# Kernel optimization log

Measured on AMD Instinct MI355X. Metric: run time of the kernel, lower is better.

## Reference

```python
import jax, jax.numpy as jnp
import numpy as np

N = 100000          # nodes
E = 1600000         # edges
NODE_DIM = 128
EDGE_DIM = 1
EMB = 16            # out_channels per head
H = 2               # heads
HID = 32
OUT = 2
NEG_SLOPE = 0.2


def gatv2_layer(x, src, dst, eattr, Wl, bl, Wr, br, We, att, bias):
    """PyG GATv2Conv: add self-loops (edge_attr fill='mean'), edge attention,
    segment softmax over target nodes, scatter-add aggregation, concat heads."""
    n = x.shape[0]
    heads, ch = att.shape
    # --- add self loops; self-loop edge_attr = mean of incoming edge_attr per node ---
    ones = jnp.ones((src.shape[0],), dtype=x.dtype)
    deg = jax.ops.segment_sum(ones, dst, num_segments=n)
    loop_attr = jax.ops.segment_sum(eattr, dst, num_segments=n) / jnp.maximum(deg, 1.0)[:, None]
    idx = jnp.arange(n, dtype=src.dtype)
    src2 = jnp.concatenate([src, idx])
    dst2 = jnp.concatenate([dst, idx])
    eattr2 = jnp.concatenate([eattr, loop_attr], axis=0)
    # --- linear projections ---
    xl = (x @ Wl + bl).reshape(n, heads, ch)   # source-side (lin_l)
    xr = (x @ Wr + br).reshape(n, heads, ch)   # target-side (lin_r)
    ef = (eattr2 @ We).reshape(-1, heads, ch)  # edge features (lin_edge, no bias)
    # --- per-edge attention logits (GATv2: LeakyReLU inside, then att dot) ---
    e = xl[src2] + xr[dst2] + ef               # [E2, H, C]
    e = jnp.where(e >= 0, e, NEG_SLOPE * e)
    logits = jnp.einsum('ehc,hc->eh', e, att)  # [E2, H]
    # --- segment softmax over edges sharing the same target node ---
    m = jax.ops.segment_max(logits, dst2, num_segments=n)      # [N, H]
    a = jnp.exp(logits - m[dst2])
    denom = jax.ops.segment_sum(a, dst2, num_segments=n)
    alpha = a / denom[dst2]                                    # [E2, H]
    # --- scatter-add weighted source messages ---
    msg = (alpha[:, :, None] * xl[src2]).reshape(-1, heads * ch)
    out = jax.ops.segment_sum(msg, dst2, num_segments=n)       # [N, H*C]
    return out + bias


def setup_inputs() -> dict:
    key = jax.random.key(0)
    ks = jax.random.split(key, 24)
    p = lambda k, s: (jax.random.normal(k, s, dtype=jnp.float32) * 0.1)
    HC = H * EMB
    return {
        'x': jax.random.normal(ks[0], (N, NODE_DIM), dtype=jnp.float32),
        'edge_index': jax.random.randint(ks[1], (2, E), 0, N, dtype=jnp.int32),
        'edge_attr': jax.random.normal(ks[2], (E, EDGE_DIM), dtype=jnp.float32),
        # layer 1
        'Wl1': p(ks[3], (NODE_DIM, HC)), 'bl1': p(ks[4], (HC,)),
        'Wr1': p(ks[5], (NODE_DIM, HC)), 'br1': p(ks[6], (HC,)),
        'We1': p(ks[7], (EDGE_DIM, HC)), 'att1': p(ks[8], (H, EMB)), 'b1': p(ks[9], (HC,)),
        # layer 2 (input dim = H*EMB)
        'Wl2': p(ks[10], (HC, HC)), 'bl2': p(ks[11], (HC,)),
        'Wr2': p(ks[12], (HC, HC)), 'br2': p(ks[13], (HC,)),
        'We2': p(ks[14], (EDGE_DIM, HC)), 'att2': p(ks[15], (H, EMB)), 'b2': p(ks[16], (HC,)),
        # decoder MLP
        'Wd1': p(ks[17], (HC, HID)), 'bd1': p(ks[18], (HID,)),
        'Wd2': p(ks[19], (HID, OUT)), 'bd2': p(ks[20], (OUT,)),
    }


def reference(x, edge_index, edge_attr,
              Wl1, bl1, Wr1, br1, We1, att1, b1,
              Wl2, bl2, Wr2, br2, We2, att2, b2,
              Wd1, bd1, Wd2, bd2):
    src, dst = edge_index[0], edge_index[1]
    h = gatv2_layer(x, src, dst, edge_attr, Wl1, bl1, Wr1, br1, We1, att1, b1)
    h = gatv2_layer(h, src, dst, edge_attr, Wl2, bl2, Wr2, br2, We2, att2, b2)
    h = jax.nn.relu(h @ Wd1 + bd1)
    return h @ Wd2 + bd2
```

## Files before the change

kernel.cpp:

```cpp
#include <hip/hip_runtime.h>
#include <hip/hip_fp16.h>
#include <math.h>


#define NN 100000
#define NE 1600000
#define SLOT 48
#define ROWU 64
#define NEG_SLOPE 0.2f

__device__ __forceinline__ float pk_ea(unsigned p) {
    return __half2float(__ushort_as_half((unsigned short)((p & 0x7FFFu) << 1)));
}
__device__ __forceinline__ float lrelu(float v) {
    return (v >= 0.f) ? v : NEG_SLOPE * v;
}

__device__ __forceinline__ void scatter_chunk(int bid, int tid,
                                              const int* __restrict__ src,
                                              const int* __restrict__ dst,
                                              const float* __restrict__ eattr,
                                              unsigned* __restrict__ csr) {
#pragma unroll
    for (int i = 0; i < 2; i++) {
        int e = bid * 512 + i * 256 + tid;
        int d = dst[e];
        unsigned* row = csr + (size_t)d * ROWU;
        int pos = atomicAdd((int*)row, 1);
        if (pos < SLOT) {
            unsigned hb = __half_as_ushort(__float2half_rn(eattr[e]));
            row[4 + pos] = ((unsigned)src[e] << 15) | (hb >> 1);
        }
    }
}

template <int K>
__global__ void proj_scatter_kernel(const float* __restrict__ x,
                                    const float* __restrict__ Wl, const float* __restrict__ bl,
                                    const float* __restrict__ Wr, const float* __restrict__ br,
                                    __half* __restrict__ xl, float* __restrict__ xr,
                                    const int* __restrict__ src, const int* __restrict__ dst,
                                    const float* __restrict__ eattr,
                                    unsigned* __restrict__ csr) {
    __shared__ __align__(16) float sWl[K * 32];
    __shared__ __align__(16) float sWr[K * 32];
    __shared__ float sb[64];
    bool scat_first = (blockIdx.x & 1) != 0;
    if (scat_first)
        scatter_chunk(blockIdx.x, threadIdx.x, src, dst, eattr, csr);
    for (int a = threadIdx.x; a < K * 32; a += blockDim.x) {
        int col = a / K, p = a % K;
        int k = (((p >> 2) ^ (col & 7)) << 2) | (p & 3);
        sWl[a] = Wl[k * 32 + col];
        sWr[a] = Wr[k * 32 + col];
    }
    if (threadIdx.x < 32) sb[threadIdx.x] = bl[threadIdx.x];
    else if (threadIdx.x < 64) sb[threadIdx.x] = br[threadIdx.x - 32];
    __syncthreads();
    int t = blockIdx.x * blockDim.x + threadIdx.x;
    int g = t >> 5, col = t & 31;
    int row0 = g * 4;
    {
        const float4* x0 = (const float4*)(x + (size_t)(row0 + 0) * K);
        const float4* x1 = (const float4*)(x + (size_t)(row0 + 1) * K);
        const float4* x2 = (const float4*)(x + (size_t)(row0 + 2) * K);
        const float4* x3 = (const float4*)(x + (size_t)(row0 + 3) * K);
        const float4* wl4 = (const float4*)(sWl + col * K);
        const float4* wr4 = (const float4*)(sWr + col * K);
        int swz = col & 7;
        float al0 = 0.f, al1 = 0.f, al2 = 0.f, al3 = 0.f;
        float ar0 = 0.f, ar1 = 0.f, ar2 = 0.f, ar3 = 0.f;
#pragma unroll 4
        for (int k4 = 0; k4 < K / 4; k4++) {
            float4 wl = wl4[k4 ^ swz];
            float4 wr = wr4[k4 ^ swz];
            float4 a = x0[k4];
            float4 b = x1[k4];
            float4 c = x2[k4];
            float4 d = x3[k4];
            al0 = fmaf(a.x, wl.x, al0); al0 = fmaf(a.y, wl.y, al0);
            al0 = fmaf(a.z, wl.z, al0); al0 = fmaf(a.w, wl.w, al0);
            ar0 = fmaf(a.x, wr.x, ar0); ar0 = fmaf(a.y, wr.y, ar0);
            ar0 = fmaf(a.z, wr.z, ar0); ar0 = fmaf(a.w, wr.w, ar0);
            al1 = fmaf(b.x, wl.x, al1); al1 = fmaf(b.y, wl.y, al1);
            al1 = fmaf(b.z, wl.z, al1); al1 = fmaf(b.w, wl.w, al1);
            ar1 = fmaf(b.x, wr.x, ar1); ar1 = fmaf(b.y, wr.y, ar1);
            ar1 = fmaf(b.z, wr.z, ar1); ar1 = fmaf(b.w, wr.w, ar1);
            al2 = fmaf(c.x, wl.x, al2); al2 = fmaf(c.y, wl.y, al2);
            al2 = fmaf(c.z, wl.z, al2); al2 = fmaf(c.w, wl.w, al2);
            ar2 = fmaf(c.x, wr.x, ar2); ar2 = fmaf(c.y, wr.y, ar2);
            ar2 = fmaf(c.z, wr.z, ar2); ar2 = fmaf(c.w, wr.w, ar2);
            al3 = fmaf(d.x, wl.x, al3); al3 = fmaf(d.y, wl.y, al3);
            al3 = fmaf(d.z, wl.z, al3); al3 = fmaf(d.w, wl.w, al3);
            ar3 = fmaf(d.x, wr.x, ar3); ar3 = fmaf(d.y, wr.y, ar3);
            ar3 = fmaf(d.w, wr.w, ar3); ar3 = fmaf(d.z, wr.z, ar3);
        }
        float bls = sb[col], brs = sb[32 + col];
        xl[(size_t)(row0 + 0) * 32 + col] = __float2half_rn(al0 + bls);
        xr[(size_t)(row0 + 0) * 32 + col] = ar0 + brs;
        xl[(size_t)(row0 + 1) * 32 + col] = __float2half_rn(al1 + bls);
        xr[(size_t)(row0 + 1) * 32 + col] = ar1 + brs;
        xl[(size_t)(row0 + 2) * 32 + col] = __float2half_rn(al2 + bls);
        xr[(size_t)(row0 + 2) * 32 + col] = ar2 + brs;
        xl[(size_t)(row0 + 3) * 32 + col] = __float2half_rn(al3 + bls);
        xr[(size_t)(row0 + 3) * 32 + col] = ar3 + brs;
    }
    if (!scat_first)
        scatter_chunk(blockIdx.x, threadIdx.x, src, dst, eattr, csr);
}

__device__ __forceinline__ void gat_core4(const unsigned* __restrict__ csr,
                                          const __half* xl, const float* xr,
                                          const float* We, const float* att,
                                          const float* bias, int node, int L,
                                          float h[4]) {
    int k = L & 7, j = L >> 3;
    const unsigned* row = csr + (size_t)node * ROWU;
    int cnt = (int)row[0];
    int deg = (cnt < SLOT) ? cnt : SLOT;
    float4 we = ((const float4*)We)[k];
    float4 at = ((const float4*)att)[k];
    float4 xrc = ((const float4*)(xr + (size_t)node * 32))[k];
    ushort4 sq = ((const ushort4*)(xl + (size_t)node * 32))[k];
    float sx0 = __half2float(__ushort_as_half(sq.x));
    float sx1 = __half2float(__ushort_as_half(sq.y));
    float sx2 = __half2float(__ushort_as_half(sq.z));
    float sx3 = __half2float(__ushort_as_half(sq.w));
    float ssum = 0.f, a0 = 0.f, a1 = 0.f, a2 = 0.f, a3 = 0.f, easum = 0.f;
    unsigned pv_c = row[4 + j];
    int n1 = j + 4; if (n1 > SLOT - 1) n1 = SLOT - 1;
    unsigned pv_n = row[4 + n1];
    bool val_c = j < deg;
    int s_c = val_c ? (int)(pv_c >> 15) : 0;
    ushort4 q_c = ((const ushort4*)(xl + (size_t)s_c * 32))[k];
    for (int base = 0; base < deg; base += 4) {
        int idx = base + j;
        bool val_n = (idx + 4) < deg;
        int s_n = val_n ? (int)(pv_n >> 15) : 0;
        ushort4 q_n = ((const ushort4*)(xl + (size_t)s_n * 32))[k];
        int n2 = idx + 8; if (n2 > SLOT - 1) n2 = SLOT - 1;
        unsigned pv_n2 = row[4 + n2];
        float ea = pk_ea(pv_c);
        float x0 = __half2float(__ushort_as_half(q_c.x));
        float x1 = __half2float(__ushort_as_half(q_c.y));
        float x2 = __half2float(__ushort_as_half(q_c.z));
        float x3 = __half2float(__ushort_as_half(q_c.w));
        float p;
        p  = at.x * lrelu(fmaf(ea, we.x, x0 + xrc.x));
        p  = fmaf(at.y, lrelu(fmaf(ea, we.y, x1 + xrc.y)), p);
        p  = fmaf(at.z, lrelu(fmaf(ea, we.z, x2 + xrc.z)), p);
        p  = fmaf(at.w, lrelu(fmaf(ea, we.w, x3 + xrc.w)), p);
        p += __shfl_xor(p, 1);
        p += __shfl_xor(p, 2);
        float w = val_c ? __expf(p) : 0.f;
        ssum += w;
        easum += val_c ? ea : 0.f;
        a0 = fmaf(w, x0, a0);
        a1 = fmaf(w, x1, a1);
        a2 = fmaf(w, x2, a2);
        a3 = fmaf(w, x3, a3);
        pv_c = pv_n; pv_n = pv_n2; q_c = q_n; val_c = val_n;
    }
    ssum  += __shfl_xor(ssum, 8);   ssum  += __shfl_xor(ssum, 16);
    easum += __shfl_xor(easum, 8);  easum += __shfl_xor(easum, 16);
    a0 += __shfl_xor(a0, 8);  a0 += __shfl_xor(a0, 16);
    a1 += __shfl_xor(a1, 8);  a1 += __shfl_xor(a1, 16);
    a2 += __shfl_xor(a2, 8);  a2 += __shfl_xor(a2, 16);
    a3 += __shfl_xor(a3, 8);  a3 += __shfl_xor(a3, 16);
    {
        float ea0 = easum / fmaxf((float)cnt, 1.f);
        float p;
        p  = at.x * lrelu(fmaf(ea0, we.x, sx0 + xrc.x));
        p  = fmaf(at.y, lrelu(fmaf(ea0, we.y, sx1 + xrc.y)), p);
        p  = fmaf(at.z, lrelu(fmaf(ea0, we.z, sx2 + xrc.z)), p);
        p  = fmaf(at.w, lrelu(fmaf(ea0, we.w, sx3 + xrc.w)), p);
        p += __shfl_xor(p, 1);
        p += __shfl_xor(p, 2);
        float w = __expf(p);
        ssum += w;
        a0 = fmaf(w, sx0, a0);
        a1 = fmaf(w, sx1, a1);
        a2 = fmaf(w, sx2, a2);
        a3 = fmaf(w, sx3, a3);
    }
    float4 bq = ((const float4*)bias)[k];
    float inv = 1.f / ssum;
    h[0] = a0 * inv + bq.x;
    h[1] = a1 * inv + bq.y;
    h[2] = a2 * inv + bq.z;
    h[3] = a3 * inv + bq.w;
}

#define HBUF_FENCE() do { \
    asm volatile("s_waitcnt lgkmcnt(0)" ::: "memory"); \
    __builtin_amdgcn_sched_barrier(0); \
} while (0)

__global__ void gat1_proj2_kernel(const unsigned* __restrict__ csr,
                                  const __half* __restrict__ xl, const float* __restrict__ xr,
                                  const float* __restrict__ We, const float* __restrict__ att,
                                  const float* __restrict__ bias,
                                  const float* __restrict__ Wl2, const float* __restrict__ bl2,
                                  const float* __restrict__ Wr2, const float* __restrict__ br2,
                                  __half* __restrict__ xl2, float* __restrict__ xr2) {
    __shared__ __align__(16) float sWl[1024];
    __shared__ __align__(16) float sWr[1024];
    __shared__ float4 hbuf[8][8];
    for (int i = threadIdx.x; i < 1024; i += blockDim.x) {
        int cc = i >> 5, Lc = i & 31;
        int p = (((cc >> 2) ^ (Lc & 7)) << 2) | (cc & 3);
        sWl[Lc * 32 + p] = Wl2[i];
        sWr[Lc * 32 + p] = Wr2[i];
    }
    __syncthreads();
    int t = blockIdx.x * blockDim.x + threadIdx.x;
    int node = t >> 5, L = t & 31;
    if (node >= NN) return;
    float h[4];
    gat_core4(csr, xl, xr, We, att, bias, node, L, h);
    int nl = threadIdx.x >> 5;
    if (L < 8) hbuf[nl][L] = make_float4(h[0], h[1], h[2], h[3]);
    HBUF_FENCE();
    const float4* hv4 = hbuf[nl];
    const float4* wl4 = (const float4*)(sWl + L * 32);
    const float4* wr4 = (const float4*)(sWr + L * 32);
    int swz = L & 7;
    float al = bl2[L], ar = br2[L];
#pragma unroll
    for (int c4 = 0; c4 < 8; c4++) {
        float4 hv = hv4[c4];
        float4 wl = wl4[c4 ^ swz];
        float4 wr = wr4[c4 ^ swz];
        al = fmaf(hv.x, wl.x, al); al = fmaf(hv.y, wl.y, al);
        al = fmaf(hv.z, wl.z, al); al = fmaf(hv.w, wl.w, al);
        ar = fmaf(hv.x, wr.x, ar); ar = fmaf(hv.y, wr.y, ar);
        ar = fmaf(hv.z, wr.z, ar); ar = fmaf(hv.w, wr.w, ar);
    }
    xl2[(size_t)node * 32 + L] = __float2half_rn(al);
    xr2[(size_t)node * 32 + L] = ar;
}

__global__ void gat2_dec_kernel(const unsigned* __restrict__ csr,
                                const __half* __restrict__ xl, const float* __restrict__ xr,
                                const float* __restrict__ We, const float* __restrict__ att,
                                const float* __restrict__ bias,
                                const float* __restrict__ Wd1, const float* __restrict__ bd1,
                                const float* __restrict__ Wd2, const float* __restrict__ bd2,
                                float* __restrict__ out) {
    __shared__ __align__(16) float sWd1[1024];
    __shared__ float sWd2[64];
    __shared__ float4 hbuf[8][8];
    for (int i = threadIdx.x; i < 1024; i += blockDim.x) {
        int cc = i >> 5, Lc = i & 31;
        int p = (((cc >> 2) ^ (Lc & 7)) << 2) | (cc & 3);
        sWd1[Lc * 32 + p] = Wd1[i];
    }
    if (threadIdx.x < 64) sWd2[threadIdx.x] = Wd2[threadIdx.x];
    __syncthreads();
    int t = blockIdx.x * blockDim.x + threadIdx.x;
    int node = t >> 5, L = t & 31;
    if (node >= NN) return;
    float h[4];
    gat_core4(csr, xl, xr, We, att, bias, node, L, h);
    int nl = threadIdx.x >> 5;
    if (L < 8) hbuf[nl][L] = make_float4(h[0], h[1], h[2], h[3]);
    HBUF_FENCE();
    const float4* hv4 = hbuf[nl];
    const float4* wd4 = (const float4*)(sWd1 + L * 32);
    int swz = L & 7;
    float d1 = bd1[L];
#pragma unroll
    for (int c4 = 0; c4 < 8; c4++) {
        float4 hv = hv4[c4];
        float4 wd = wd4[c4 ^ swz];
        d1 = fmaf(hv.x, wd.x, d1); d1 = fmaf(hv.y, wd.y, d1);
        d1 = fmaf(hv.z, wd.z, d1); d1 = fmaf(hv.w, wd.w, d1);
    }
    float hid = fmaxf(d1, 0.f);
    float o0 = hid * sWd2[L * 2 + 0];
    float o1 = hid * sWd2[L * 2 + 1];
    o0 += __shfl_xor(o0, 1);   o1 += __shfl_xor(o1, 1);
    o0 += __shfl_xor(o0, 2);   o1 += __shfl_xor(o1, 2);
    o0 += __shfl_xor(o0, 4);   o1 += __shfl_xor(o1, 4);
    o0 += __shfl_xor(o0, 8);   o1 += __shfl_xor(o1, 8);
    o0 += __shfl_xor(o0, 16);  o1 += __shfl_xor(o1, 16);
    if (L == 0) {
        out[(size_t)node * 2 + 0] = o0 + bd2[0];
        out[(size_t)node * 2 + 1] = o1 + bd2[1];
    }
}

extern "C" void kernel_launch(void* const* d_in, const int* in_sizes, int n_in,
                              void* d_out, int out_size, void* d_ws, size_t ws_size,
                              hipStream_t stream) {
    const float* x     = (const float*)d_in[0];
    const int*   src   = (const int*)d_in[1];
    const int*   dst   = src + NE;
    const float* eattr = (const float*)d_in[2];
    const float* Wl1 = (const float*)d_in[3],  *bl1 = (const float*)d_in[4];
    const float* Wr1 = (const float*)d_in[5],  *br1 = (const float*)d_in[6];
    const float* We1 = (const float*)d_in[7],  *att1 = (const float*)d_in[8];
    const float* b1  = (const float*)d_in[9];
    const float* Wl2 = (const float*)d_in[10], *bl2 = (const float*)d_in[11];
    const float* Wr2 = (const float*)d_in[12], *br2 = (const float*)d_in[13];
    const float* We2 = (const float*)d_in[14], *att2 = (const float*)d_in[15];
    const float* b2  = (const float*)d_in[16];
    const float* Wd1 = (const float*)d_in[17], *bd1 = (const float*)d_in[18];
    const float* Wd2 = (const float*)d_in[19], *bd2 = (const float*)d_in[20];
    float* out = (float*)d_out;

    char* w = (char*)d_ws;
    unsigned* csr = (unsigned*)w;  w += (size_t)NN * ROWU * 4;
    __half*   xl  = (__half*)w;    w += (size_t)NN * 32 * 2;
    float*    xr  = (float*)w;     w += (size_t)NN * 32 * 4;
    __half*   xl2 = (__half*)w;    w += (size_t)NN * 32 * 2;
    float*    xr2 = (float*)w;     w += (size_t)NN * 32 * 4;

    const int B = 256;
    const int gN32 = (NN * 32) / B;
    const int gP   = (NN / 4 * 32) / B;

    hipMemsetAsync(csr, 0, (size_t)NN * ROWU * 4, stream);

    proj_scatter_kernel<128><<<gP, B, 0, stream>>>(x, Wl1, bl1, Wr1, br1, xl, xr,
                                                   src, dst, eattr, csr);

    gat1_proj2_kernel<<<gN32, B, 0, stream>>>(csr, xl, xr, We1, att1, b1,
                                              Wl2, bl2, Wr2, br2, xl2, xr2);

    gat2_dec_kernel<<<gN32, B, 0, stream>>>(csr, xl2, xr2, We2, att2, b2,
                                            Wd1, bd1, Wd2, bd2, out);
}
```

Measured before the change: 390.1 us.

## Use full 64-lane wave per node in first GAT layer aggregation

The first GAT layer now assigns 64 lanes per node instead of 32, so eight edges are processed in parallel per iteration with prefetching of the next source rows. The second-layer projection is split so half the wave computes lin_l and half lin_r. The projection kernel also always runs the edge scatter after the matmul and replaces div/mod with shifts. This aims to raise memory-level parallelism on the gather-heavy aggregation, at the cost of more shuffle reductions and fewer nodes per block.

```diff
diff --git a/kernel.cpp b/kernel.cpp
--- a/kernel.cpp
+++ b/kernel.cpp
@@ -45,11 +45,8 @@
     __shared__ __align__(16) float sWl[K * 32];
     __shared__ __align__(16) float sWr[K * 32];
     __shared__ float sb[64];
-    bool scat_first = (blockIdx.x & 1) != 0;
-    if (scat_first)
-        scatter_chunk(blockIdx.x, threadIdx.x, src, dst, eattr, csr);
     for (int a = threadIdx.x; a < K * 32; a += blockDim.x) {
-        int col = a / K, p = a % K;
+        int col = a >> 7, p = a & (K - 1);
         int k = (((p >> 2) ^ (col & 7)) << 2) | (p & 3);
         sWl[a] = Wl[k * 32 + col];
         sWr[a] = Wr[k * 32 + col];
@@ -105,8 +102,89 @@
         xl[(size_t)(row0 + 3) * 32 + col] = __float2half_rn(al3 + bls);
         xr[(size_t)(row0 + 3) * 32 + col] = ar3 + brs;
     }
-    if (!scat_first)
-        scatter_chunk(blockIdx.x, threadIdx.x, src, dst, eattr, csr);
+    scatter_chunk(blockIdx.x, threadIdx.x, src, dst, eattr, csr);
+}
+
+__device__ __forceinline__ void gat_core8(const unsigned* __restrict__ csr,
+                                          const __half* xl, const float* xr,
+                                          const float* We, const float* att,
+                                          const float* bias, int node, int L,
+                                          float h[4]) {
+    int k = L & 7, j = L >> 3;
+    const unsigned* row = csr + (size_t)node * ROWU;
+    int cnt = (int)row[0];
+    int deg = (cnt < SLOT) ? cnt : SLOT;
+    float4 we = ((const float4*)We)[k];
+    float4 at = ((const float4*)att)[k];
+    float4 xrc = ((const float4*)(xr + (size_t)node * 32))[k];
+    ushort4 sq = ((const ushort4*)(xl + (size_t)node * 32))[k];
+    float sx0 = __half2float(__ushort_as_half(sq.x));
+    float sx1 = __half2float(__ushort_as_half(sq.y));
+    float sx2 = __half2float(__ushort_as_half(sq.z));
+    float sx3 = __half2float(__ushort_as_half(sq.w));
+    float ssum = 0.f, a0 = 0.f, a1 = 0.f, a2 = 0.f, a3 = 0.f, easum = 0.f;
+    unsigned pv_c = row[4 + j];
+    int n1 = j + 8; if (n1 > SLOT - 1) n1 = SLOT - 1;
+    unsigned pv_n = row[4 + n1];
+    bool val_c = j < deg;
+    int s_c = val_c ? (int)(pv_c >> 15) : 0;
+    ushort4 q_c = ((const ushort4*)(xl + (size_t)s_c * 32))[k];
+    for (int base = 0; base < deg; base += 8) {
+        int idx = base + j;
+        bool val_n = (idx + 8) < deg;
+        int s_n = val_n ? (int)(pv_n >> 15) : 0;
+        ushort4 q_n = ((const ushort4*)(xl + (size_t)s_n * 32))[k];
+        int n2 = idx + 16; if (n2 > SLOT - 1) n2 = SLOT - 1;
+        unsigned pv_n2 = row[4 + n2];
+        float ea = pk_ea(pv_c);
+        float x0 = __half2float(__ushort_as_half(q_c.x));
+        float x1 = __half2float(__ushort_as_half(q_c.y));
+        float x2 = __half2float(__ushort_as_half(q_c.z));
+        float x3 = __half2float(__ushort_as_half(q_c.w));
+        float p;
+        p  = at.x * lrelu(fmaf(ea, we.x, x0 + xrc.x));
+        p  = fmaf(at.y, lrelu(fmaf(ea, we.y, x1 + xrc.y)), p);
+        p  = fmaf(at.z, lrelu(fmaf(ea, we.z, x2 + xrc.z)), p);
+        p  = fmaf(at.w, lrelu(fmaf(ea, we.w, x3 + xrc.w)), p);
+        p += __shfl_xor(p, 1);
+        p += __shfl_xor(p, 2);
+        float w = val_c ? __expf(p) : 0.f;
+        ssum += w;
+        easum += val_c ? ea : 0.f;
+        a0 = fmaf(w, x0, a0);
+        a1 = fmaf(w, x1, a1);
+        a2 = fmaf(w, x2, a2);
+        a3 = fmaf(w, x3, a3);
+        pv_c = pv_n; pv_n = pv_n2; q_c = q_n; val_c = val_n;
+    }
+    ssum  += __shfl_xor(ssum, 8);   ssum  += __shfl_xor(ssum, 16);  ssum  += __shfl_xor(ssum, 32);
+    easum += __shfl_xor(easum, 8);  easum += __shfl_xor(easum, 16); easum += __shfl_xor(easum, 32);
+    a0 += __shfl_xor(a0, 8);  a0 += __shfl_xor(a0, 16);  a0 += __shfl_xor(a0, 32);
+    a1 += __shfl_xor(a1, 8);  a1 += __shfl_xor(a1, 16);  a1 += __shfl_xor(a1, 32);
+    a2 += __shfl_xor(a2, 8);  a2 += __shfl_xor(a2, 16);  a2 += __shfl_xor(a2, 32);
+    a3 += __shfl_xor(a3, 8);  a3 += __shfl_xor(a3, 16);  a3 += __shfl_xor(a3, 32);
+    {
+        float ea0 = easum / fmaxf((float)cnt, 1.f);
+        float p;
+        p  = at.x * lrelu(fmaf(ea0, we.x, sx0 + xrc.x));
+        p  = fmaf(at.y, lrelu(fmaf(ea0, we.y, sx1 + xrc.y)), p);
+        p  = fmaf(at.z, lrelu(fmaf(ea0, we.z, sx2 + xrc.z)), p);
+        p  = fmaf(at.w, lrelu(fmaf(ea0, we.w, sx3 + xrc.w)), p);
+        p += __shfl_xor(p, 1);
+        p += __shfl_xor(p, 2);
+        float w = __expf(p);
+        ssum += w;
+        a0 = fmaf(w, sx0, a0);
+        a1 = fmaf(w, sx1, a1);
+        a2 = fmaf(w, sx2, a2);
+        a3 = fmaf(w, sx3, a3);
+    }
+    float4 bq = ((const float4*)bias)[k];
+    float inv = 1.f / ssum;
+    h[0] = a0 * inv + bq.x;
+    h[1] = a1 * inv + bq.y;
+    h[2] = a2 * inv + bq.z;
+    h[3] = a3 * inv + bq.w;
 }
 
 __device__ __forceinline__ void gat_core4(const unsigned* __restrict__ csr,
@@ -205,7 +283,7 @@
                                   __half* __restrict__ xl2, float* __restrict__ xr2) {
     __shared__ __align__(16) float sWl[1024];
     __shared__ __align__(16) float sWr[1024];
-    __shared__ float4 hbuf[8][8];
+    __shared__ float4 hbuf[4][8];
     for (int i = threadIdx.x; i < 1024; i += blockDim.x) {
         int cc = i >> 5, Lc = i & 31;
         int p = (((cc >> 2) ^ (Lc & 7)) << 2) | (cc & 3);
@@ -214,30 +292,27 @@
     }
     __syncthreads();
     int t = blockIdx.x * blockDim.x + threadIdx.x;
-    int node = t >> 5, L = t & 31;
-    if (node >= NN) return;
+    int node = t >> 6, L = t & 63;
     float h[4];
-    gat_core4(csr, xl, xr, We, att, bias, node, L, h);
-    int nl = threadIdx.x >> 5;
+    gat_core8(csr, xl, xr, We, att, bias, node, L, h);
+    int nl = threadIdx.x >> 6;
     if (L < 8) hbuf[nl][L] = make_float4(h[0], h[1], h[2], h[3]);
     HBUF_FENCE();
     const float4* hv4 = hbuf[nl];
-    const float4* wl4 = (const float4*)(sWl + L * 32);
-    const float4* wr4 = (const float4*)(sWr + L * 32);
-    int swz = L & 7;
-    float al = bl2[L], ar = br2[L];
+    int c = L & 31, half = L >> 5;
+    const float* wsel = half ? sWr : sWl;
+    const float4* w4 = (const float4*)(wsel + c * 32);
+    int swz = c & 7;
+    float acc = half ? br2[c] : bl2[c];
 #pragma unroll
     for (int c4 = 0; c4 < 8; c4++) {
         float4 hv = hv4[c4];
-        float4 wl = wl4[c4 ^ swz];
-        float4 wr = wr4[c4 ^ swz];
-        al = fmaf(hv.x, wl.x, al); al = fmaf(hv.y, wl.y, al);
-        al = fmaf(hv.z, wl.z, al); al = fmaf(hv.w, wl.w, al);
-        ar = fmaf(hv.x, wr.x, ar); ar = fmaf(hv.y, wr.y, ar);
-        ar = fmaf(hv.z, wr.z, ar); ar = fmaf(hv.w, wr.w, ar);
-    }
-    xl2[(size_t)node * 32 + L] = __float2half_rn(al);
-    xr2[(size_t)node * 32 + L] = ar;
+        float4 wv = w4[c4 ^ swz];
+        acc = fmaf(hv.x, wv.x, acc); acc = fmaf(hv.y, wv.y, acc);
+        acc = fmaf(hv.z, wv.z, acc); acc = fmaf(hv.w, wv.w, acc);
+    }
+    if (half == 0) xl2[(size_t)node * 32 + c] = __float2half_rn(acc);
+    else           xr2[(size_t)node * 32 + c] = acc;
 }
 
 __global__ void gat2_dec_kernel(const unsigned* __restrict__ csr,
@@ -317,17 +392,18 @@
     float*    xr2 = (float*)w;     w += (size_t)NN * 32 * 4;
 
     const int B = 256;
-    const int gN32 = (NN * 32) / B;
     const int gP   = (NN / 4 * 32) / B;
+    const int gG1  = NN / 4;
+    const int gG2  = (NN * 32) / B;
 
     hipMemsetAsync(csr, 0, (size_t)NN * ROWU * 4, stream);
 
     proj_scatter_kernel<128><<<gP, B, 0, stream>>>(x, Wl1, bl1, Wr1, br1, xl, xr,
                                                    src, dst, eattr, csr);
 
-    gat1_proj2_kernel<<<gN32, B, 0, stream>>>(csr, xl, xr, We1, att1, b1,
-                                              Wl2, bl2, Wr2, br2, xl2, xr2);
-
-    gat2_dec_kernel<<<gN32, B, 0, stream>>>(csr, xl2, xr2, We2, att2, b2,
-                                            Wd1, bd1, Wd2, bd2, out);
-}
+    gat1_proj2_kernel<<<gG1, B, 0, stream>>>(csr, xl, xr, We1, att1, b1,
+                                             Wl2, bl2, Wr2, br2, xl2, xr2);
+
+    gat2_dec_kernel<<<gG2, B, 0, stream>>>(csr, xl2, xr2, We2, att2, b2,
+                                           Wd1, bd1, Wd2, bd2, out);
+}
```

After: 423.0 us. 1.08x slower.
